# Optimization experiments

Hardware: AMD Instinct MI355X
Metric: run time of the kernel (lower is better)

## Reference

```python
import jax, jax.numpy as jnp
import numpy as np

N = 100000
F_IN = 166
HID = 128
HEADS = 4
OUT = HID // HEADS  # 32
E = 1600000
NEG_SLOPE = 0.2


def setup_inputs() -> dict:
    key = jax.random.key(0)
    ks = jax.random.split(key, 12)
    x = jax.random.normal(ks[0], (N, F_IN), dtype=jnp.float32)
    edge_index = jax.random.randint(ks[1], (2, E), 0, N, dtype=jnp.int64)
    # xavier_uniform with gain=0.1 as in _init_weights
    def xavier(k, shape, gain=0.1):
        fan_in, fan_out = shape[0], shape[1]
        a = gain * np.sqrt(6.0 / (fan_in + fan_out))
        return jax.random.uniform(k, shape, jnp.float32, -a, a)
    W_in = xavier(ks[2], (F_IN, HID))
    b_in = jnp.zeros((HID,), jnp.float32)
    W_gat = xavier(ks[3], (HID, HEADS * OUT), gain=1.0)
    att_src = jax.random.normal(ks[4], (HEADS, OUT), jnp.float32) * 0.1
    att_dst = jax.random.normal(ks[5], (HEADS, OUT), jnp.float32) * 0.1
    b_gat = jnp.zeros((HEADS * OUT,), jnp.float32)
    W1 = xavier(ks[6], (HID, 64))
    b1 = jnp.zeros((64,), jnp.float32)
    W2 = xavier(ks[7], (64, 2))
    b2 = jnp.zeros((2,), jnp.float32)
    return {"x": x, "edge_index": edge_index, "W_in": W_in, "b_in": b_in,
            "W_gat": W_gat, "att_src": att_src, "att_dst": att_dst, "b_gat": b_gat,
            "W1": W1, "b1": b1, "W2": W2, "b2": b2}


def _gat_layer(h, src, dst, W_gat, att_src, att_dst, b_gat):
    # h: [N, HID]; src/dst: [E'] (self-loops included)
    n = h.shape[0]
    hW = (h @ W_gat).reshape(n, HEADS, OUT)          # [N, H, O]
    a_src = jnp.einsum('nho,ho->nh', hW, att_src)     # [N, H]
    a_dst = jnp.einsum('nho,ho->nh', hW, att_dst)
    e = a_src[src] + a_dst[dst]                       # [E, H]
    e = jnp.where(e > 0, e, NEG_SLOPE * e)            # leaky_relu(0.2)
    # segment softmax over destination nodes
    m = jax.ops.segment_max(e, dst, num_segments=n)   # [N, H]
    m = jnp.where(jnp.isfinite(m), m, 0.0)
    ex = jnp.exp(e - m[dst])
    s = jax.ops.segment_sum(ex, dst, num_segments=n)  # [N, H]
    alpha = ex / (s[dst] + 1e-16)                     # [E, H]
    msg = hW[src] * alpha[:, :, None]                 # [E, H, O]
    out = jax.ops.segment_sum(msg, dst, num_segments=n)
    return out.reshape(n, HEADS * OUT) + b_gat


def reference(x, edge_index, W_in, b_in, W_gat, att_src, att_dst, b_gat, W1, b1, W2, b2):
    n = x.shape[0]
    # input projection + relu
    h = jax.nn.relu(x @ W_in + b_in)
    # PyG GATConv adds self-loops by default
    loops = jnp.arange(n, dtype=edge_index.dtype)
    src = jnp.concatenate([edge_index[0], loops])
    dst = jnp.concatenate([edge_index[1], loops])
    h = _gat_layer(h, src, dst, W_gat, att_src, att_dst, b_gat)
    # dropout is identity in eval mode
    h = jax.nn.relu(h @ W1 + b1)
    logits = h @ W2 + b2
    return logits
```

## Files before the change

### kernel.cpp

```cpp
#include <hip/hip_runtime.h>
#include <hip/hip_fp16.h>

#define DEVFN __device__ __forceinline__

constexpr int N    = 100000;
constexpr int F_IN = 166;
constexpr int HID  = 128;
constexpr int E    = 1600000;

using half8 = __attribute__((ext_vector_type(8))) _Float16;
using f32x4 = __attribute__((ext_vector_type(4))) float;

constexpr size_t HW_OFF   = 0;
constexpr size_t GOUT_OFF = 25600000;
constexpr size_t ASRC_OFF = 51200000;
constexpr size_t ADST_OFF = 52800000;
constexpr size_t ROW_OFF  = 54800000;
constexpr size_t BCNT_OFF = 55200016;
constexpr size_t WPK1_OFF = 55600544;
constexpr size_t WPK2_OFF = 55649696;
constexpr size_t WPK3_OFF = 55682464;
constexpr size_t CSR_OFF  = 55700000;

constexpr int PROJ_ROWS  = 64;
constexpr int PROJ_NB    = (N + PROJ_ROWS - 1) / PROJ_ROWS;
constexpr int MLP_NB     = (N + 63) / 64;
constexpr int EPB        = 1024;

constexpr int NBUCK     = 49;
constexpr int BCAP      = 40960;

DEVFN float lrelu(float e) { return e > 0.0f ? e : 0.2f * e; }

DEVFN void acc8h(const float4& q, const float x, float4& a0, float4& a1)
{
    const __half2* h = (const __half2*)&q;
    a0.x = fmaf(__low2float(h[0]),  x, a0.x);
    a0.y = fmaf(__high2float(h[0]), x, a0.y);
    a0.z = fmaf(__low2float(h[1]),  x, a0.z);
    a0.w = fmaf(__high2float(h[1]), x, a0.w);
    a1.x = fmaf(__low2float(h[2]),  x, a1.x);
    a1.y = fmaf(__high2float(h[2]), x, a1.y);
    a1.z = fmaf(__low2float(h[3]),  x, a1.z);
    a1.w = fmaf(__high2float(h[3]), x, a1.w);
}

__global__ __launch_bounds__(256) void k_prep(const float* __restrict__ Win,
                                              const float* __restrict__ Wgat,
                                              const float* __restrict__ W1,
                                              __half* __restrict__ Wpk1,
                                              __half* __restrict__ Wpk2,
                                              __half* __restrict__ Wpk3,
                                              int* __restrict__ bcnt)
{
    const int idx = blockIdx.x * 256 + threadIdx.x;
    if (idx < NBUCK) bcnt[idx] = 0;
    if (idx < 24576) {
        const int i  = idx & 7;
        const int l  = (idx >> 3) & 63;
        const int tt = (idx >> 9) & 7;
        const int ks = idx >> 12;
        const int k   = ks * 32 + (l >> 4) * 8 + i;
        const int col = tt * 16 + (l & 15);
        const float v = (k < F_IN) ? Win[k * HID + col] : 0.0f;
        Wpk1[idx] = __float2half(v);
    } else if (idx < 40960) {
        const int j  = idx - 24576;
        const int i  = j & 7;
        const int l  = (j >> 3) & 63;
        const int tt = (j >> 9) & 7;
        const int ks = j >> 12;
        const int k   = ks * 32 + (l >> 4) * 8 + i;
        const int col = tt * 16 + (l & 15);
        Wpk2[j] = __float2half(Wgat[k * HID + col]);
    } else {
        const int j  = idx - 40960;
        const int i  = j & 7;
        const int l  = (j >> 3) & 63;
        const int tt = (j >> 9) & 3;
        const int ks = j >> 11;
        const int k   = ks * 32 + (l >> 4) * 8 + i;
        const int col = tt * 16 + (l & 15);
        Wpk3[j] = __float2half(W1[k * 64 + col]);
    }
}

__global__ __launch_bounds__(256) void k_proj(
    const float* __restrict__ x,
    const __half* __restrict__ Wpk1, const __half* __restrict__ Wpk2,
    const float* __restrict__ bin,
    const float* __restrict__ attS, const float* __restrict__ attD,
    __half* __restrict__ hWh, float* __restrict__ aS, float* __restrict__ aD,
    const int* __restrict__ ei, int* __restrict__ bcnt,
    int* __restrict__ interm)
{
    __shared__ __align__(16) __half sh[PROJ_ROWS * 200];

    const int t    = threadIdx.x;
    const int row0 = blockIdx.x * PROJ_ROWS;
    const int w    = t >> 6;
    const int lane = t & 63;
    const int l15  = lane & 15;
    const int g    = lane >> 4;
    const int arow = w * 16 + l15;

    for (int idx = t; idx < PROJ_ROWS * 100; idx += 256) {
        const int r   = idx / 100;
        const int kk2 = (idx - r * 100) * 2;
        float2 v = make_float2(0.f, 0.f);
        const int row = row0 + r;
        if (row < N && kk2 < F_IN)
            v = *(const float2*)&x[(size_t)row * F_IN + kk2];
        *(__half2*)&sh[r * 200 + kk2] = __float22half2_rn(v);
    }
    __syncthreads();

    f32x4 acc[8];
#pragma unroll
    for (int tt = 0; tt < 8; ++tt)
#pragma unroll
        for (int q = 0; q < 4; ++q) acc[tt][q] = 0.0f;

#pragma unroll
    for (int ks = 0; ks < 6; ++ks) {
        const half8 a = *(const half8*)&sh[arow * 200 + ks * 32 + g * 8];
        const half8* bp = (const half8*)&Wpk1[ks * 4096 + lane * 8];
#pragma unroll
        for (int tt = 0; tt < 8; ++tt) {
            acc[tt] = __builtin_amdgcn_mfma_f32_16x16x32_f16(a, bp[tt * 64], acc[tt], 0, 0, 0);
        }
    }

    __syncthreads();

#pragma unroll
    for (int tt = 0; tt < 8; ++tt) {
        const int col = tt * 16 + l15;
        const float bv = bin[col];
#pragma unroll
        for (int rg = 0; rg < 4; ++rg) {
            const int r = w * 16 + g * 4 + rg;
            sh[r * 136 + col] = __float2half(fmaxf(acc[tt][rg] + bv, 0.0f));
        }
    }
    __syncthreads();

#pragma unroll
    for (int tt = 0; tt < 8; ++tt)
#pragma unroll
        for (int q = 0; q < 4; ++q) acc[tt][q] = 0.0f;

#pragma unroll
    for (int ks = 0; ks < 4; ++ks) {
        const half8 a = *(const half8*)&sh[arow * 136 + ks * 32 + g * 8];
        const half8* bp = (const half8*)&Wpk2[ks * 4096 + lane * 8];
#pragma unroll
        for (int tt = 0; tt < 8; ++tt) {
            acc[tt] = __builtin_amdgcn_mfma_f32_16x16x32_f16(a, bp[tt * 64], acc[tt], 0, 0, 0);
        }
    }

    const int grow0 = row0 + w * 16 + g * 4;
    float asv[8], adv[8];
#pragma unroll
    for (int tt = 0; tt < 8; ++tt) {
        asv[tt] = attS[tt * 16 + l15];
        adv[tt] = attD[tt * 16 + l15];
    }
    float psb[4][4], pdb[4][4];
#pragma unroll
    for (int rg = 0; rg < 4; ++rg) {
#pragma unroll
        for (int h = 0; h < 4; ++h) {
            float ps = acc[2*h][rg] * asv[2*h] + acc[2*h+1][rg] * asv[2*h+1];
            float pd = acc[2*h][rg] * adv[2*h] + acc[2*h+1][rg] * adv[2*h+1];
#pragma unroll
            for (int off = 1; off <= 8; off <<= 1) {
                ps += __shfl_xor(ps, off);
                pd += __shfl_xor(pd, off);
            }
            psb[rg][h] = ps; pdb[rg][h] = pd;
        }
    }
    if (l15 == 0) {
#pragma unroll
        for (int rg = 0; rg < 4; ++rg) {
            const int row = grow0 + rg;
            if (row < N) {
                *(float4*)&aS[row * 4] = make_float4(psb[rg][0], psb[rg][1], psb[rg][2], psb[rg][3]);
                *(float4*)&aD[row * 4] = make_float4(pdb[rg][0], pdb[rg][1], pdb[rg][2], pdb[rg][3]);
            }
        }
    }

    __syncthreads();
#pragma unroll
    for (int tt = 0; tt < 8; ++tt) {
        const int col = tt * 16 + l15;
#pragma unroll
        for (int rg = 0; rg < 4; ++rg) {
            const int r = w * 16 + g * 4 + rg;
            sh[r * 136 + col] = __float2half(acc[tt][rg]);
        }
    }
    __syncthreads();
    for (int idx = t; idx < PROJ_ROWS * 16; idx += 256) {
        const int r  = idx >> 4;
        const int c8 = idx & 15;
        const int row = row0 + r;
        if (row < N) {
            const uint4 v = *(const uint4*)&sh[r * 136 + c8 * 8];
            *(uint4*)&hWh[(size_t)row * HID + c8 * 8] = v;
        }
    }

    __syncthreads();
    int* hist  = (int*)sh;
    int* basep = hist + 64;
    int* offp  = hist + 128;
    if (t < NBUCK) hist[t] = 0;
    __syncthreads();

    const int e0 = blockIdx.x * EPB;
    int pk[4], bk[4];
#pragma unroll
    for (int j = 0; j < 4; ++j) {
        const int i = e0 + j * 256 + t;
        bk[j] = -1;
        if (i < E) {
            const int s = ei[i], d = ei[E + i];
            const int b = d >> 11;
            bk[j] = b;
            pk[j] = s | ((d & 2047) << 17);
            atomicAdd(&hist[b], 1);
        }
    }
    __syncthreads();
    if (t < NBUCK) { basep[t] = atomicAdd(&bcnt[t], hist[t]); offp[t] = 0; }
    __syncthreads();
#pragma unroll
    for (int j = 0; j < 4; ++j) {
        if (bk[j] >= 0) {
            const int p   = atomicAdd(&offp[bk[j]], 1);
            const int pos = basep[bk[j]] + p;
            if (pos < BCAP) interm[bk[j] * BCAP + pos] = pk[j];
        }
    }
}

__global__ __launch_bounds__(256) void k_binB(const int* __restrict__ interm,
                                              const int* __restrict__ bcnt,
                                              int* __restrict__ rowstart,
                                              int* __restrict__ csr)
{
    __shared__ int cnt[2048];
    __shared__ int wsum[256];
    __shared__ int sbase;
    const int t      = threadIdx.x;
    const int bucket = blockIdx.x;

    if (t < 64) {
        int v = (t < NBUCK && t < bucket) ? min(bcnt[t], BCAP) : 0;
#pragma unroll
        for (int off = 32; off >= 1; off >>= 1) v += __shfl_xor(v, off);
        if (t == 0) sbase = v;
    }
    if (bucket == 0 && t == 0) rowstart[N] = E;
    for (int i = t; i < 2048; i += 256) cnt[i] = 0;
    __syncthreads();

    const int total = min(bcnt[bucket], BCAP);
    const int beg   = bucket * BCAP;
    for (int i = beg + t; i < beg + total; i += 256)
        atomicAdd(&cnt[interm[i] >> 17], 1);
    __syncthreads();

    int loc[8];
    int s = 0;
#pragma unroll
    for (int j = 0; j < 8; ++j) { loc[j] = cnt[t * 8 + j]; s += loc[j]; }
    wsum[t] = s;
    __syncthreads();
    for (int off = 1; off < 256; off <<= 1) {
        const int v = (t >= off) ? wsum[t - off] : 0;
        __syncthreads();
        wsum[t] += v;
        __syncthreads();
    }
    int run = sbase + wsum[t] - s;
#pragma unroll
    for (int j = 0; j < 8; ++j) {
        cnt[t * 8 + j] = run;
        const int node = bucket * 2048 + t * 8 + j;
        if (node < N) rowstart[node] = run;
        run += loc[j];
    }
    __syncthreads();

    for (int i = beg + t; i < beg + total; i += 256) {
        const int p   = interm[i];
        const int pos = atomicAdd(&cnt[p >> 17], 1);
        csr[pos] = p & 0x1FFFF;
    }
}

__global__ __launch_bounds__(256) void k_agg(
    const int* __restrict__ rowstart, const int* __restrict__ csr,
    const float* __restrict__ aS, const float* __restrict__ aD,
    const __half* __restrict__ hWh, const float4* __restrict__ bgat4,
    __half* __restrict__ gout)
{
    const int t = threadIdx.x;
    const int w = t >> 6;
    const int n = blockIdx.x * 4 + w;
    const int lane = t & 63;
    const int slot = lane >> 4;
    const int cg   = lane & 15;
    const int head = cg >> 2;

    const int r0 = rowstart[n], r1 = rowstart[n + 1];
    const float adh = aD[n * 4 + head];

    float4 a0 = {0.f,0.f,0.f,0.f}, a1 = {0.f,0.f,0.f,0.f};
    float ss = 0.0f;

    if (slot == 0) {
        const float x0 = __expf(lrelu(aS[n * 4 + head] + adh));
        const float4 q = *(const float4*)&hWh[(size_t)n * HID + cg * 8];
        acc8h(q, x0, a0, a1);
        ss += x0;
    }

    int j = r0 + slot;
    for (; j + 4 < r1; j += 8) {
        const int s0 = csr[j], s1 = csr[j + 4];
        const float x0 = __expf(lrelu(aS[s0 * 4 + head] + adh));
        const float x1 = __expf(lrelu(aS[s1 * 4 + head] + adh));
        const float4 q0 = *(const float4*)&hWh[(size_t)s0 * HID + cg * 8];
        const float4 q1 = *(const float4*)&hWh[(size_t)s1 * HID + cg * 8];
        acc8h(q0, x0, a0, a1);
        acc8h(q1, x1, a0, a1);
        ss += x0 + x1;
    }
    if (j < r1) {
        const int s0 = csr[j];
        const float x0 = __expf(lrelu(aS[s0 * 4 + head] + adh));
        const float4 q = *(const float4*)&hWh[(size_t)s0 * HID + cg * 8];
        acc8h(q, x0, a0, a1);
        ss += x0;
    }

#pragma unroll
    for (int off = 16; off <= 32; off <<= 1) {
        a0.x += __shfl_xor(a0.x, off); a0.y += __shfl_xor(a0.y, off);
        a0.z += __shfl_xor(a0.z, off); a0.w += __shfl_xor(a0.w, off);
        a1.x += __shfl_xor(a1.x, off); a1.y += __shfl_xor(a1.y, off);
        a1.z += __shfl_xor(a1.z, off); a1.w += __shfl_xor(a1.w, off);
        ss += __shfl_xor(ss, off);
    }

    if (slot == 0) {
        const float inv = 1.0f / (ss + 1e-16f);
        const float4 bg0 = bgat4[cg * 2 + 0];
        const float4 bg1 = bgat4[cg * 2 + 1];
        const __half2 h0 = __float22half2_rn(make_float2(a0.x*inv+bg0.x, a0.y*inv+bg0.y));
        const __half2 h1 = __float22half2_rn(make_float2(a0.z*inv+bg0.z, a0.w*inv+bg0.w));
        const __half2 h2 = __float22half2_rn(make_float2(a1.x*inv+bg1.x, a1.y*inv+bg1.y));
        const __half2 h3 = __float22half2_rn(make_float2(a1.z*inv+bg1.z, a1.w*inv+bg1.w));
        uint4 p;
        p.x = *(const unsigned*)&h0; p.y = *(const unsigned*)&h1;
        p.z = *(const unsigned*)&h2; p.w = *(const unsigned*)&h3;
        *(uint4*)&gout[(size_t)n * HID + cg * 8] = p;
    }
}

__global__ __launch_bounds__(256) void k_mlp(
    const __half* __restrict__ gout, const __half* __restrict__ Wpk3,
    const float* __restrict__ b1, const float* __restrict__ W2,
    const float* __restrict__ b2, float2* __restrict__ out)
{
    const int t = threadIdx.x;
    const int w = t >> 6, lane = t & 63;
    const int l15 = lane & 15, g = lane >> 4;
    const int rowbase = blockIdx.x * 64 + w * 16;
    const int arow = rowbase + l15;
    const bool arok = (arow < N);

    f32x4 acc[4];
#pragma unroll
    for (int tt = 0; tt < 4; ++tt)
#pragma unroll
        for (int q = 0; q < 4; ++q) acc[tt][q] = 0.0f;

#pragma unroll
    for (int ks = 0; ks < 4; ++ks) {
        half8 a;
#pragma unroll
        for (int i = 0; i < 8; ++i) a[i] = (_Float16)0;
        if (arok) a = *(const half8*)&gout[(size_t)arow * HID + ks * 32 + g * 8];
        const half8* bp = (const half8*)&Wpk3[ks * 2048 + lane * 8];
#pragma unroll
        for (int tt = 0; tt < 4; ++tt)
            acc[tt] = __builtin_amdgcn_mfma_f32_16x16x32_f16(a, bp[tt * 64], acc[tt], 0, 0, 0);
    }

    float l0[4] = {0.f, 0.f, 0.f, 0.f}, l1[4] = {0.f, 0.f, 0.f, 0.f};
#pragma unroll
    for (int tt = 0; tt < 4; ++tt) {
        const int col = tt * 16 + l15;
        const float bv = b1[col];
        const float2 wv = *(const float2*)&W2[col * 2];
#pragma unroll
        for (int rg = 0; rg < 4; ++rg) {
            const float h2 = fmaxf(acc[tt][rg] + bv, 0.0f);
            l0[rg] = fmaf(h2, wv.x, l0[rg]);
            l1[rg] = fmaf(h2, wv.y, l1[rg]);
        }
    }
#pragma unroll
    for (int off = 1; off <= 8; off <<= 1) {
#pragma unroll
        for (int rg = 0; rg < 4; ++rg) {
            l0[rg] += __shfl_xor(l0[rg], off);
            l1[rg] += __shfl_xor(l1[rg], off);
        }
    }
    if (l15 == 0) {
        const float b20 = b2[0], b21 = b2[1];
#pragma unroll
        for (int rg = 0; rg < 4; ++rg) {
            const int row = rowbase + g * 4 + rg;
            if (row < N) out[row] = make_float2(l0[rg] + b20, l1[rg] + b21);
        }
    }
}

extern "C" void kernel_launch(void* const* d_in, const int* in_sizes, int n_in,
                              void* d_out, int out_size, void* d_ws, size_t ws_size,
                              hipStream_t stream) {
    const float* x     = (const float*)d_in[0];
    const int*   ei    = (const int*)d_in[1];
    const float* Win   = (const float*)d_in[2];
    const float* bin   = (const float*)d_in[3];
    const float* Wgat  = (const float*)d_in[4];
    const float* attS  = (const float*)d_in[5];
    const float* attD  = (const float*)d_in[6];
    const float* bgat  = (const float*)d_in[7];
    const float* W1    = (const float*)d_in[8];
    const float* b1    = (const float*)d_in[9];
    const float* W2    = (const float*)d_in[10];
    const float* b2    = (const float*)d_in[11];

    char* ws = (char*)d_ws;
    __half* hWh   = (__half*)(ws + HW_OFF);
    __half* gout  = (__half*)(ws + GOUT_OFF);
    int*   interm = (int*)(ws + GOUT_OFF);
    float* aS     = (float*)(ws + ASRC_OFF);
    float* aD     = (float*)(ws + ADST_OFF);
    int*   row    = (int*)(ws + ROW_OFF);
    int*   bcnt   = (int*)(ws + BCNT_OFF);
    __half* Wpk1  = (__half*)(ws + WPK1_OFF);
    __half* Wpk2  = (__half*)(ws + WPK2_OFF);
    __half* Wpk3  = (__half*)(ws + WPK3_OFF);
    int*   csr    = (int*)(ws + CSR_OFF);

    k_prep<<<192, 256, 0, stream>>>(Win, Wgat, W1, Wpk1, Wpk2, Wpk3, bcnt);
    k_proj<<<PROJ_NB, 256, 0, stream>>>(x, Wpk1, Wpk2, bin, attS, attD,
                                        hWh, aS, aD, ei, bcnt, interm);
    k_binB<<<NBUCK, 256, 0, stream>>>(interm, bcnt, row, csr);
    k_agg<<<N / 4, 256, 0, stream>>>(row, csr, aS, aD, hWh,
                                     (const float4*)bgat, gout);
    k_mlp<<<MLP_NB, 256, 0, stream>>>(gout, Wpk3, b1, W2, b2, (float2*)d_out);
}
```

Measured before the change: 344.2 us.

## Widen projection and binning blocks to split columns across more waves

Doubles k_proj to 512 threads, with each wave computing half of the output columns for 16 rows, so each thread needs fewer accumulator registers and more waves run in parallel. Attention logits are now computed from the fp16 tile in shared memory instead of through register shuffles. k_binB grows to 1024 threads per bucket, giving more parallelism for counting and scattering at the cost of a longer block-wide scan. The attention dot products now read rounded fp16 values, which slightly changes numerics.

```diff
diff --git a/kernel.cpp b/kernel.cpp
--- a/kernel.cpp
+++ b/kernel.cpp
@@ -85,7 +85,7 @@
     }
 }
 
-__global__ __launch_bounds__(256) void k_proj(
+__global__ __launch_bounds__(512) void k_proj(
     const float* __restrict__ x,
     const __half* __restrict__ Wpk1, const __half* __restrict__ Wpk2,
     const float* __restrict__ bin,
@@ -102,9 +102,11 @@
     const int lane = t & 63;
     const int l15  = lane & 15;
     const int g    = lane >> 4;
-    const int arow = w * 16 + l15;
-
-    for (int idx = t; idx < PROJ_ROWS * 100; idx += 256) {
+    const int rg4  = w & 3;
+    const int cgr  = w >> 2;
+    const int arow = rg4 * 16 + l15;
+
+    for (int idx = t; idx < PROJ_ROWS * 100; idx += 512) {
         const int r   = idx / 100;
         const int kk2 = (idx - r * 100) * 2;
         float2 v = make_float2(0.f, 0.f);
@@ -115,18 +117,18 @@
     }
     __syncthreads();
 
-    f32x4 acc[8];
-#pragma unroll
-    for (int tt = 0; tt < 8; ++tt)
+    f32x4 acc[4];
+#pragma unroll
+    for (int tt = 0; tt < 4; ++tt)
 #pragma unroll
         for (int q = 0; q < 4; ++q) acc[tt][q] = 0.0f;
 
 #pragma unroll
     for (int ks = 0; ks < 6; ++ks) {
         const half8 a = *(const half8*)&sh[arow * 200 + ks * 32 + g * 8];
-        const half8* bp = (const half8*)&Wpk1[ks * 4096 + lane * 8];
-#pragma unroll
-        for (int tt = 0; tt < 8; ++tt) {
+        const half8* bp = (const half8*)&Wpk1[ks * 4096 + cgr * 2048 + lane * 8];
+#pragma unroll
+        for (int tt = 0; tt < 4; ++tt) {
             acc[tt] = __builtin_amdgcn_mfma_f32_16x16x32_f16(a, bp[tt * 64], acc[tt], 0, 0, 0);
         }
     }
@@ -134,77 +136,67 @@
     __syncthreads();
 
 #pragma unroll
-    for (int tt = 0; tt < 8; ++tt) {
-        const int col = tt * 16 + l15;
+    for (int tt = 0; tt < 4; ++tt) {
+        const int col = (cgr * 4 + tt) * 16 + l15;
         const float bv = bin[col];
 #pragma unroll
         for (int rg = 0; rg < 4; ++rg) {
-            const int r = w * 16 + g * 4 + rg;
+            const int r = rg4 * 16 + g * 4 + rg;
             sh[r * 136 + col] = __float2half(fmaxf(acc[tt][rg] + bv, 0.0f));
         }
     }
     __syncthreads();
 
 #pragma unroll
-    for (int tt = 0; tt < 8; ++tt)
+    for (int tt = 0; tt < 4; ++tt)
 #pragma unroll
         for (int q = 0; q < 4; ++q) acc[tt][q] = 0.0f;
 
 #pragma unroll
     for (int ks = 0; ks < 4; ++ks) {
         const half8 a = *(const half8*)&sh[arow * 136 + ks * 32 + g * 8];
-        const half8* bp = (const half8*)&Wpk2[ks * 4096 + lane * 8];
-#pragma unroll
-        for (int tt = 0; tt < 8; ++tt) {
+        const half8* bp = (const half8*)&Wpk2[ks * 4096 + cgr * 2048 + lane * 8];
+#pragma unroll
+        for (int tt = 0; tt < 4; ++tt) {
             acc[tt] = __builtin_amdgcn_mfma_f32_16x16x32_f16(a, bp[tt * 64], acc[tt], 0, 0, 0);
         }
     }
 
-    const int grow0 = row0 + w * 16 + g * 4;
-    float asv[8], adv[8];
-#pragma unroll
-    for (int tt = 0; tt < 8; ++tt) {
-        asv[tt] = attS[tt * 16 + l15];
-        adv[tt] = attD[tt * 16 + l15];
-    }
-    float psb[4][4], pdb[4][4];
-#pragma unroll
-    for (int rg = 0; rg < 4; ++rg) {
-#pragma unroll
-        for (int h = 0; h < 4; ++h) {
-            float ps = acc[2*h][rg] * asv[2*h] + acc[2*h+1][rg] * asv[2*h+1];
-            float pd = acc[2*h][rg] * adv[2*h] + acc[2*h+1][rg] * adv[2*h+1];
-#pragma unroll
-            for (int off = 1; off <= 8; off <<= 1) {
-                ps += __shfl_xor(ps, off);
-                pd += __shfl_xor(pd, off);
-            }
-            psb[rg][h] = ps; pdb[rg][h] = pd;
-        }
-    }
-    if (l15 == 0) {
+    __syncthreads();
+#pragma unroll
+    for (int tt = 0; tt < 4; ++tt) {
+        const int col = (cgr * 4 + tt) * 16 + l15;
 #pragma unroll
         for (int rg = 0; rg < 4; ++rg) {
-            const int row = grow0 + rg;
-            if (row < N) {
-                *(float4*)&aS[row * 4] = make_float4(psb[rg][0], psb[rg][1], psb[rg][2], psb[rg][3]);
-                *(float4*)&aD[row * 4] = make_float4(pdb[rg][0], pdb[rg][1], pdb[rg][2], pdb[rg][3]);
-            }
-        }
-    }
-
-    __syncthreads();
-#pragma unroll
-    for (int tt = 0; tt < 8; ++tt) {
-        const int col = tt * 16 + l15;
-#pragma unroll
-        for (int rg = 0; rg < 4; ++rg) {
-            const int r = w * 16 + g * 4 + rg;
+            const int r = rg4 * 16 + g * 4 + rg;
             sh[r * 136 + col] = __float2half(acc[tt][rg]);
         }
     }
     __syncthreads();
-    for (int idx = t; idx < PROJ_ROWS * 16; idx += 256) {
+
+    {
+        const int r2   = t >> 3;
+        const int c8   = t & 7;
+        const int head = c8 >> 1;
+        float ps = 0.0f, pd = 0.0f;
+#pragma unroll
+        for (int k2 = 0; k2 < 8; ++k2) {
+            const int col = c8 * 16 + k2 * 2;
+            const __half2 hv = *(const __half2*)&sh[r2 * 136 + col];
+            const float v0 = __low2float(hv), v1 = __high2float(hv);
+            ps = fmaf(v0, attS[col], fmaf(v1, attS[col + 1], ps));
+            pd = fmaf(v0, attD[col], fmaf(v1, attD[col + 1], pd));
+        }
+        ps += __shfl_xor(ps, 1);
+        pd += __shfl_xor(pd, 1);
+        const int row = row0 + r2;
+        if (!(c8 & 1) && row < N) {
+            aS[row * 4 + head] = ps;
+            aD[row * 4 + head] = pd;
+        }
+    }
+
+    for (int idx = t; idx < PROJ_ROWS * 16; idx += 512) {
         const int r  = idx >> 4;
         const int c8 = idx & 15;
         const int row = row0 + r;
@@ -222,10 +214,10 @@
     __syncthreads();
 
     const int e0 = blockIdx.x * EPB;
-    int pk[4], bk[4];
-#pragma unroll
-    for (int j = 0; j < 4; ++j) {
-        const int i = e0 + j * 256 + t;
+    int pk[2], bk[2];
+#pragma unroll
+    for (int j = 0; j < 2; ++j) {
+        const int i = e0 + j * 512 + t;
         bk[j] = -1;
         if (i < E) {
             const int s = ei[i], d = ei[E + i];
@@ -239,7 +231,7 @@
     if (t < NBUCK) { basep[t] = atomicAdd(&bcnt[t], hist[t]); offp[t] = 0; }
     __syncthreads();
 #pragma unroll
-    for (int j = 0; j < 4; ++j) {
+    for (int j = 0; j < 2; ++j) {
         if (bk[j] >= 0) {
             const int p   = atomicAdd(&offp[bk[j]], 1);
             const int pos = basep[bk[j]] + p;
@@ -248,13 +240,13 @@
     }
 }
 
-__global__ __launch_bounds__(256) void k_binB(const int* __restrict__ interm,
-                                              const int* __restrict__ bcnt,
-                                              int* __restrict__ rowstart,
-                                              int* __restrict__ csr)
+__global__ __launch_bounds__(1024) void k_binB(const int* __restrict__ interm,
+                                               const int* __restrict__ bcnt,
+                                               int* __restrict__ rowstart,
+                                               int* __restrict__ csr)
 {
     __shared__ int cnt[2048];
-    __shared__ int wsum[256];
+    __shared__ int wsum[1024];
     __shared__ int sbase;
     const int t      = threadIdx.x;
     const int bucket = blockIdx.x;
@@ -266,38 +258,37 @@
         if (t == 0) sbase = v;
     }
     if (bucket == 0 && t == 0) rowstart[N] = E;
-    for (int i = t; i < 2048; i += 256) cnt[i] = 0;
+    for (int i = t; i < 2048; i += 1024) cnt[i] = 0;
     __syncthreads();
 
     const int total = min(bcnt[bucket], BCAP);
     const int beg   = bucket * BCAP;
-    for (int i = beg + t; i < beg + total; i += 256)
+    for (int i = beg + t; i < beg + total; i += 1024)
         atomicAdd(&cnt[interm[i] >> 17], 1);
     __syncthreads();
 
-    int loc[8];
-    int s = 0;
-#pragma unroll
-    for (int j = 0; j < 8; ++j) { loc[j] = cnt[t * 8 + j]; s += loc[j]; }
+    const int l0 = cnt[t * 2], l1 = cnt[t * 2 + 1];
+    const int s  = l0 + l1;
     wsum[t] = s;
     __syncthreads();
-    for (int off = 1; off < 256; off <<= 1) {
+    for (int off = 1; off < 1024; off <<= 1) {
         const int v = (t >= off) ? wsum[t - off] : 0;
         __syncthreads();
         wsum[t] += v;
         __syncthreads();
     }
     int run = sbase + wsum[t] - s;
-#pragma unroll
-    for (int j = 0; j < 8; ++j) {
-        cnt[t * 8 + j] = run;
-        const int node = bucket * 2048 + t * 8 + j;
+    {
+        const int node = bucket * 2048 + t * 2;
+        cnt[t * 2] = run;
         if (node < N) rowstart[node] = run;
-        run += loc[j];
-    }
-    __syncthreads();
-
-    for (int i = beg + t; i < beg + total; i += 256) {
+        run += l0;
+        cnt[t * 2 + 1] = run;
+        if (node + 1 < N) rowstart[node + 1] = run;
+    }
+    __syncthreads();
+
+    for (int i = beg + t; i < beg + total; i += 1024) {
         const int p   = interm[i];
         const int pos = atomicAdd(&cnt[p >> 17], 1);
         csr[pos] = p & 0x1FFFF;
@@ -465,9 +456,9 @@
     int*   csr    = (int*)(ws + CSR_OFF);
 
     k_prep<<<192, 256, 0, stream>>>(Win, Wgat, W1, Wpk1, Wpk2, Wpk3, bcnt);
-    k_proj<<<PROJ_NB, 256, 0, stream>>>(x, Wpk1, Wpk2, bin, attS, attD,
+    k_proj<<<PROJ_NB, 512, 0, stream>>>(x, Wpk1, Wpk2, bin, attS, attD,
                                         hWh, aS, aD, ei, bcnt, interm);
-    k_binB<<<NBUCK, 256, 0, stream>>>(interm, bcnt, row, csr);
+    k_binB<<<NBUCK, 1024, 0, stream>>>(interm, bcnt, row, csr);
     k_agg<<<N / 4, 256, 0, stream>>>(row, csr, aS, aD, hWh,
                                      (const float4*)bgat, gout);
     k_mlp<<<MLP_NB, 256, 0, stream>>>(gout, Wpk3, b1, W2, b2, (float2*)d_out);
```

New measurement: 280.5 us. 18.5% less time.
